# Optimization experiments

Hardware: AMD Instinct MI355X
Metric: run time of the kernel (lower is better)

Reference implementation:

```python
import jax, jax.numpy as jnp
import numpy as np

HID = 128
N_BLOCKS = 50000
ATOMS_PER_BLOCK = 8
N_ATOMS = N_BLOCKS * ATOMS_PER_BLOCK  # 400k
N_EDGES = 800000
ATOM_VOCAB = 100
N_BOND_TYPES = 5
CORRUPT_RATIO = 0.1


def setup_inputs() -> dict:
    key = jax.random.key(0)
    ks = jax.random.split(key, 20)
    A = jax.random.randint(ks[0], (N_ATOMS,), 0, ATOM_VOCAB)
    src = jax.random.randint(ks[1], (N_EDGES,), 0, N_ATOMS)
    dst = jax.random.randint(ks[2], (N_EDGES,), 0, N_ATOMS)
    btyp = jax.random.randint(ks[3], (N_EDGES,), 0, N_BOND_TYPES)
    bonds = jnp.stack([src, dst, btyp], axis=1)  # [E, 3]
    block_ids = jnp.arange(N_ATOMS) // ATOMS_PER_BLOCK  # atom -> block, sorted
    generate_mask = jax.random.uniform(ks[4], (N_BLOCKS,)) < 0.5
    position_ids = jax.random.randint(ks[5], (N_BLOCKS,), 0, 1024)
    is_aa = jax.random.randint(ks[6], (N_BLOCKS,), 0, 2)
    corrupt_rand = jax.random.uniform(ks[7], (N_BLOCKS,))
    s = 0.02
    p = {
        'atom_embed': jax.random.normal(ks[8], (ATOM_VOCAB, HID)) * s,
        'bond_embed': jax.random.normal(ks[9], (N_BOND_TYPES, HID)) * s,
        'is_aa_embed': jax.random.normal(ks[10], (2, HID)) * s,
        'gine_w1': jax.random.normal(ks[11], (HID, HID)) * s,
        'gine_b1': jnp.zeros((HID,)),
        'gine_w2': jax.random.normal(ks[12], (HID, HID)) * s,
        'gine_b2': jnp.zeros((HID,)),
        'mlp_w0': jax.random.normal(ks[13], (3 * HID, HID)) * s,
        'mlp_b0': jnp.zeros((HID,)),
        'mlp_w1': jax.random.normal(ks[14], (HID, HID)) * s,
        'mlp_b1': jnp.zeros((HID,)),
        'mlp_w2': jax.random.normal(ks[15], (HID, HID)) * s,
        'mlp_b2': jnp.zeros((HID,)),
    }
    return dict(A=A, bonds=bonds, block_ids=block_ids, generate_mask=generate_mask,
                position_ids=position_ids, is_aa=is_aa, corrupt_rand=corrupt_rand, **p)


def _sinusoidal(pos, dim):
    # standard sinusoidal position embedding, [N] -> [N, dim]
    inv_freq = 1.0 / (10000.0 ** (jnp.arange(0, dim, 2, dtype=jnp.float32) / dim))
    ang = pos.astype(jnp.float32)[:, None] * inv_freq[None, :]
    return jnp.concatenate([jnp.sin(ang), jnp.cos(ang)], axis=-1)


def reference(A, bonds, block_ids, generate_mask, position_ids, is_aa, corrupt_rand,
              atom_embed, bond_embed, is_aa_embed,
              gine_w1, gine_b1, gine_w2, gine_b2,
              mlp_w0, mlp_b0, mlp_w1, mlp_b1, mlp_w2, mlp_b2):
    src, dst, btyp = bonds[:, 0], bonds[:, 1], bonds[:, 2]
    # context atoms: atoms whose block is NOT being generated
    ctx = ~generate_mask[block_ids]                       # [N_atoms]
    valid = (ctx[src] & ctx[dst]).astype(jnp.float32)     # edge-select mask (== dropping bonds)
    # GINEConv: msg = relu(x_j + e), aggregated by sum at dst, eps = 0
    Hn = atom_embed[A]                                    # [N_atoms, H]
    edge_attr = bond_embed[btyp]                          # [E, H]
    msg = jax.nn.relu(Hn[src] + edge_attr) * valid[:, None]
    agg = jax.ops.segment_sum(msg, dst, num_segments=N_ATOMS)
    h = Hn + agg
    h = jax.nn.relu(h @ gine_w1 + gine_b1) @ gine_w2 + gine_b2
    # std-conserving scatter mean: sum / sqrt(count)
    blk_sum = jax.ops.segment_sum(h, block_ids, num_segments=N_BLOCKS)
    cnt = jax.ops.segment_sum(jnp.ones((N_ATOMS,), jnp.float32), block_ids, num_segments=N_BLOCKS)
    topo = blk_sum / jnp.sqrt(jnp.maximum(cnt, 1.0))[:, None]
    topo = jnp.where(generate_mask[:, None], 0.0, topo)
    # is_aa embedding with corruption on generated blocks
    corrupt = generate_mask & (corrupt_rand < CORRUPT_RATIO)
    is_aa_e = is_aa_embed[jnp.where(corrupt, 0, is_aa)]
    pos_e = _sinusoidal(position_ids, HID)
    x = jnp.concatenate([pos_e, topo, is_aa_e], axis=-1)  # [N_blocks, 3H]
    # 3-layer cond MLP (dropout inactive in eval)
    x = jax.nn.relu(x @ mlp_w0 + mlp_b0)
    x = jax.nn.relu(x @ mlp_w1 + mlp_b1)
    cond = x @ mlp_w2 + mlp_b2
    return cond
```

## Files before the change

kernel.cpp:

```cpp
#include <hip/hip_runtime.h>
#include <hip/hip_bf16.h>

#define NBLK  50000
#define NATOM 400000
#define NEDGE 800000
#define CAP   40

typedef __bf16 bf16x8 __attribute__((ext_vector_type(8)));
typedef float  f32x4  __attribute__((ext_vector_type(4)));

#define MCNT_OFF 0UL
#define EW1_OFF  200000UL
#define REC_OFF  251200UL
#define T_OFF    4251200UL
#define PW_OFF   4507200UL
#define W2T_OFF  4769344UL
#define M1T_OFF  4802112UL
#define M2T_OFF  4834880UL
#define AAW_OFF  4867648UL
#define GM_OFF   4869696UL
#define FLAG_OFF 4919696UL
#define TOPO_OFF 4919712UL
#define WS_NEED  18403840UL

#define RS8 0.35355339059327373f

#define MFMA(a,b,c) __builtin_amdgcn_mfma_f32_16x16x32_bf16((a),(b),(c),0,0,0)

__device__ inline f32x4 splat4(float v){ f32x4 r; r[0]=v; r[1]=v; r[2]=v; r[3]=v; return r; }
__device__ inline float scrub(float v){ return (v==v && v<1e30f && v>-1e30f) ? v : 0.f; }

__global__ void k_sniff(const void* gm_raw, char* ws) {
  __shared__ int big;
  if (threadIdx.x == 0) big = 0;
  __syncthreads();
  const unsigned* gw = (const unsigned*)gm_raw;
  for (int i = threadIdx.x; i < 12500; i += 256)
    if (gw[i] > 1u) big = 1;
  __syncthreads();
  if (threadIdx.x == 0) *(int*)(ws + FLAG_OFF) = big;
}

__global__ void k_prep(const float* atom_embed, const float* bond_embed,
                       const float* m0, const float* m1, const float* m2,
                       const float* g2, const float* gb2, const float* aa_embed,
                       const void* gm_raw, const int* __restrict__ bonds,
                       const int* __restrict__ A, char* ws) {
  int b = blockIdx.x, t = threadIdx.x;
  if (b < 100) {
    float ae = atom_embed[b*128 + t];
    float* T = (float*)(ws + T_OFF);
    for (int bo = 0; bo < 5; ++bo) {
      float v = ae + bond_embed[bo*128 + t];
      T[(b*5 + bo)*128 + t] = v > 0.f ? v : 0.f;
    }
  } else if (b < 116) {
    int wb = b - 100;
    const float* src; __bf16* dst; int r0;
    if (wb < 8) { src = m1; dst = (__bf16*)(ws + M1T_OFF); r0 = wb*16; }
    else        { src = m2; dst = (__bf16*)(ws + M2T_OFF); r0 = (wb-8)*16; }
    for (int rr = 0; rr < 16; ++rr) {
      int r = r0 + rr;
      dst[t*128 + r] = (__bf16)src[r*128 + t];
    }
  } else if (b < 166) {
    int anyBig = *(const int*)(ws + FLAG_OFF);
    int base = (b - 116) * 1000;
    unsigned char* gu = (unsigned char*)(ws + GM_OFF);
    if (anyBig) {
      const unsigned char* gb = (const unsigned char*)gm_raw;
      for (int i = t; i < 1000; i += 128) gu[base+i] = gb[base+i] ? 1 : 0;
    } else {
      const int* gi = (const int*)gm_raw;
      for (int i = t; i < 1000; i += 128) gu[base+i] = gi[base+i] ? 1 : 0;
    }
  } else if (b < 1190) {
    int p = b - 166;
    __shared__ float s[128];
    int c = t & 63;
    float invf = exp2f((float)c * -0.20762050593046012f);
    float ang = (float)p * invf;
    s[t] = (t < 64) ? __sinf(ang) : __cosf(ang);
    __syncthreads();
    float acc = 0.f;
    #pragma unroll 4
    for (int j = 0; j < 128; ++j) acc += s[j] * m0[j*128 + t];
    ((__bf16*)(ws + PW_OFF))[p*128 + t] = (__bf16)acc;
  } else if (b < 1318) {
    int r = b - 1190;
    float acc = 0.f;
    #pragma unroll 4
    for (int j = 0; j < 128; ++j) acc += g2[r*128 + j] * m0[(128+j)*128 + t];
    ((__bf16*)(ws + W2T_OFF))[t*128 + r] = (__bf16)(acc * RS8);
  } else if (b < 1322) {
    int sf = b - 1318, sel = sf & 1, f = sf >> 1;
    float acc = 0.f;
    #pragma unroll 4
    for (int j = 0; j < 128; ++j) acc += aa_embed[sel*128 + j] * m0[(256+j)*128 + t];
    if (f) {
      float cacc = 0.f;
      #pragma unroll 4
      for (int j = 0; j < 128; ++j) cacc += gb2[j] * m0[(128+j)*128 + t];
      acc += 8.0f * RS8 * cacc;
    }
    ((float*)(ws + AAW_OFF))[sf*128 + t] = acc;
  } else {
    int anyBig = *(const int*)(ws + FLAG_OFF);
    const unsigned char* g8 = (const unsigned char*)gm_raw;
    const int* g32 = (const int*)gm_raw;
    long base = ((long)(b - 1322)*128 + t)*8;
    #pragma unroll 2
    for (int h = 0; h < 2; ++h) {
      long e4 = base + h*4;
      if (e4 >= NEDGE) break;
      const int4* bp = (const int4*)(bonds + e4*3);
      int4 w0 = bp[0], w1 = bp[1], w2 = bp[2];
      int srcs[4] = {w0.x, w0.w, w1.z, w2.y};
      int dsts[4] = {w0.y, w1.x, w1.w, w2.z};
      int bts[4]  = {w0.z, w1.y, w2.x, w2.w};
      #pragma unroll
      for (int i = 0; i < 4; ++i) {
        int sm_ = srcs[i] >> 3, dm = dsts[i] >> 3;
        int bad = anyBig ? ((int)g8[sm_] | (int)g8[dm]) : (g32[sm_] | g32[dm]);
        if (bad) continue;
        int slot = atomicAdd((int*)(ws + MCNT_OFF) + dm, 1);
        if (slot >= 0 && slot < CAP)
          ((unsigned short*)(ws + REC_OFF))[dm*CAP + slot] =
            (unsigned short)((A[srcs[i]]*5 + bts[i])*8 + (dsts[i] & 7));
      }
    }
  }
}

__global__ void k_prep2(const float* atom_embed, const float* g1, const float* gb1,
                        char* ws) {
  int b = blockIdx.x, t = threadIdx.x;
  float s0 = 0.f, s1 = 0.f, s2 = 0.f, s3 = 0.f;
  const float* row = (b < 100) ? (atom_embed + b*128) : ((float*)(ws + T_OFF) + (b-100)*128);
  #pragma unroll 4
  for (int k = 0; k < 128; k += 4) {
    s0 += row[k+0] * g1[(k+0)*128 + t];
    s1 += row[k+1] * g1[(k+1)*128 + t];
    s2 += row[k+2] * g1[(k+2)*128 + t];
    s3 += row[k+3] * g1[(k+3)*128 + t];
  }
  float s = (s0 + s1) + (s2 + s3);
  if (b < 100) {
    ((float*)(ws + EW1_OFF))[b*128 + t] = s + gb1[t];
  } else {
    __syncthreads();
    ((float*)(ws + T_OFF))[(b-100)*128 + t] = s;
  }
}

__launch_bounds__(256, 6)
__global__ void k_gather5(char* ws, const int* __restrict__ A) {
  const int tid = threadIdx.x;
  const int lane = tid & 63, wid = tid >> 6;
  const int mol = blockIdx.x*4 + wid;
  const int a_l = lane >> 3, q8 = lane & 7;
  const unsigned char* gm = (const unsigned char*)(ws + GM_OFF);

  f32x4 a0 = splat4(0.f), a1 = splat4(0.f), a2 = splat4(0.f), a3 = splat4(0.f);
  f32x4 b0 = splat4(0.f), b1 = splat4(0.f), b2 = splat4(0.f), b3 = splat4(0.f);
  if (!gm[mol]) {
    const int* cnt = (const int*)(ws + MCNT_OFF);
    const unsigned* rec32 = (const unsigned*)(ws + REC_OFF);
    const unsigned short* rec16 = (const unsigned short*)(ws + REC_OFF);
    const float* EW1 = (const float*)(ws + EW1_OFF);
    const float* TW1 = (const float*)(ws + T_OFF);
    int n = cnt[mol];
    if (n > CAP) n = CAP;
    if (n < 0) n = 0;
    int aT = A[mol*8 + a_l];
    const f32x4* ep = (const f32x4*)(EW1 + aT*128 + q8*16);
    a0 = ep[0]; a1 = ep[1]; a2 = ep[2]; a3 = ep[3];
    const int base32 = mol*(CAP/2);
    int i = 0;
    for (; i + 4 <= n; i += 4) {
      unsigned pr0 = rec32[base32 + (i >> 1)];
      unsigned pr1 = rec32[base32 + (i >> 1) + 1];
      int rv0 = pr0 & 0xFFFF, rv1 = pr0 >> 16;
      int rv2 = pr1 & 0xFFFF, rv3 = pr1 >> 16;
      int p0 = rv0 >> 3, p1 = rv1 >> 3, p2 = rv2 >> 3, p3 = rv3 >> 3;
      if (p0 < 500 && (rv0 & 7) == a_l) {
        const f32x4* tp = (const f32x4*)(TW1 + p0*128 + q8*16);
        a0 += tp[0]; a1 += tp[1]; a2 += tp[2]; a3 += tp[3];
      }
      if (p1 < 500 && (rv1 & 7) == a_l) {
        const f32x4* tp = (const f32x4*)(TW1 + p1*128 + q8*16);
        b0 += tp[0]; b1 += tp[1]; b2 += tp[2]; b3 += tp[3];
      }
      if (p2 < 500 && (rv2 & 7) == a_l) {
        const f32x4* tp = (const f32x4*)(TW1 + p2*128 + q8*16);
        a0 += tp[0]; a1 += tp[1]; a2 += tp[2]; a3 += tp[3];
      }
      if (p3 < 500 && (rv3 & 7) == a_l) {
        const f32x4* tp = (const f32x4*)(TW1 + p3*128 + q8*16);
        b0 += tp[0]; b1 += tp[1]; b2 += tp[2]; b3 += tp[3];
      }
    }
    for (; i < n; ++i) {
      int rv = rec16[mol*CAP + i];
      int p = rv >> 3;
      if (p < 500 && (rv & 7) == a_l) {
        const f32x4* tp = (const f32x4*)(TW1 + p*128 + q8*16);
        b0 += tp[0]; b1 += tp[1]; b2 += tp[2]; b3 += tp[3];
      }
    }
  }
  #pragma unroll
  for (int k = 0; k < 4; ++k) {
    float x0 = fmaxf(a0[k] + b0[k], 0.f), x1 = fmaxf(a1[k] + b1[k], 0.f);
    float x2 = fmaxf(a2[k] + b2[k], 0.f), x3 = fmaxf(a3[k] + b3[k], 0.f);
    x0 += __shfl_xor(x0, 8);  x1 += __shfl_xor(x1, 8);
    x2 += __shfl_xor(x2, 8);  x3 += __shfl_xor(x3, 8);
    x0 += __shfl_xor(x0, 16); x1 += __shfl_xor(x1, 16);
    x2 += __shfl_xor(x2, 16); x3 += __shfl_xor(x3, 16);
    x0 += __shfl_xor(x0, 32); x1 += __shfl_xor(x1, 32);
    x2 += __shfl_xor(x2, 32); x3 += __shfl_xor(x3, 32);
    a0[k] = x0; a1[k] = x1; a2[k] = x2; a3[k] = x3;
  }
  if (a_l == 0) {
    bf16x8 o0, o1;
    #pragma unroll
    for (int k = 0; k < 4; ++k) {
      o0[k] = (__bf16)a0[k]; o0[k+4] = (__bf16)a1[k];
      o1[k] = (__bf16)a2[k]; o1[k+4] = (__bf16)a3[k];
    }
    char* dst = ws + TOPO_OFF + (long)mol*256 + q8*32;
    *(bf16x8*)dst = o0;
    *(bf16x8*)(dst + 16) = o1;
  }
}

__device__ inline void gemm4(const char* sm, int aoff, const __bf16* wt,
                             const float* bias, int lane, int wave, f32x4 acc[4][2]) {
  const int colA = wave*32 + (lane & 15);
  const int k0   = (lane >> 4) * 8;
  float bb0 = bias[colA], bb1 = bias[colA + 16];
  #pragma unroll
  for (int m = 0; m < 4; ++m) { acc[m][0] = splat4(bb0); acc[m][1] = splat4(bb1); }
  #pragma unroll
  for (int kb = 0; kb < 4; ++kb) {
    bf16x8 b0 = *(const bf16x8*)(wt + colA*128 + kb*32 + k0);
    bf16x8 b1 = *(const bf16x8*)(wt + (colA+16)*128 + kb*32 + k0);
    #pragma unroll
    for (int m = 0; m < 4; ++m) {
      int rA = m*16 + (lane & 15);
      int byte = aoff + rA*256 + (((kb*64) + k0*2) ^ ((rA & 7) << 4));
      bf16x8 a = *(const bf16x8*)(sm + byte);
      acc[m][0] = MFMA(a, b0, acc[m][0]);
      acc[m][1] = MFMA(a, b1, acc[m][1]);
    }
  }
}

__device__ inline void stor4(char* sm, int off, f32x4 acc[4][2],
                             int lane, int wave, bool do_relu) {
  #pragma unroll
  for (int m = 0; m < 4; ++m)
  #pragma unroll
  for (int nf = 0; nf < 2; ++nf)
  #pragma unroll
  for (int r = 0; r < 4; ++r) {
    float v = acc[m][nf][r];
    if (do_relu && v < 0.f) v = 0.f;
    int row = m*16 + (lane >> 4)*4 + r;
    int col = wave*32 + nf*16 + (lane & 15);
    int byte = off + row*256 + ((col*2) ^ ((row & 7) << 4));
    *(__bf16*)(sm + byte) = (__bf16)v;
  }
}

__launch_bounds__(256)
__global__ void k_mlp3(char* ws, const int* __restrict__ pos_ids,
                       const int* __restrict__ is_aa, const float* cr,
                       const float* mb0, const float* mb1, const float* mb2,
                       float* __restrict__ out) {
  __shared__ __align__(16) char sm[32768];
  const int tid = threadIdx.x, lane = tid & 63, wave = tid >> 6;
  const int r0 = blockIdx.x * 64;
  const unsigned char* gm = (const unsigned char*)(ws + GM_OFF);
  const __bf16* topo_pre = (const __bf16*)(ws + TOPO_OFF);

  for (int i = 0; i < 4; ++i) {
    int idx = tid + i*256;
    int row = idx >> 4, c = idx & 15;
    int mol = r0 + row;
    bf16x8 v;
    #pragma unroll
    for (int j = 0; j < 8; ++j) v[j] = (__bf16)0.f;
    if (mol < NBLK) v = *(const bf16x8*)(topo_pre + (long)mol*128 + c*8);
    int byte = row*256 + ((c*16) ^ ((row & 7) << 4));
    *(bf16x8*)(sm + byte) = v;
  }
  if (tid < 64) {
    int mol = r0 + tid, packed = 0;
    if (mol < NBLK) {
      int g = gm[mol];
      int corrupt = g && (cr[mol] < 0.1f);
      int sel = corrupt ? 0 : is_aa[mol];
      packed = pos_ids[mol] | (sel << 12) | ((g ? 0 : 1) << 13);
    }
    *(int*)(sm + 16384 + tid*4) = packed;
  }
  __syncthreads();

  f32x4 acc[4][2];
  gemm4(sm, 0, (const __bf16*)(ws + W2T_OFF), mb0, lane, wave, acc);
  {
    const __bf16* PW = (const __bf16*)(ws + PW_OFF);
    const float* AAW = (const float*)(ws + AAW_OFF);
    #pragma unroll
    for (int m = 0; m < 4; ++m)
    #pragma unroll
    for (int r = 0; r < 4; ++r) {
      int row = m*16 + (lane >> 4)*4 + r;
      int packed = *(const int*)(sm + 16384 + row*4);
      int pid = packed & 0xFFF, sf = (packed >> 12) & 3;
      #pragma unroll
      for (int nf = 0; nf < 2; ++nf) {
        int col = wave*32 + nf*16 + (lane & 15);
        float v = acc[m][nf][r] + (float)PW[pid*128 + col] + AAW[sf*128 + col];
        acc[m][nf][r] = fmaxf(v, 0.f);
      }
    }
  }
  __syncthreads();
  stor4(sm, 0, acc, lane, wave, false);
  __syncthreads();

  gemm4(sm, 0, (const __bf16*)(ws + M1T_OFF), mb1, lane, wave, acc);
  stor4(sm, 16384, acc, lane, wave, true);
  __syncthreads();

  gemm4(sm, 16384, (const __bf16*)(ws + M2T_OFF), mb2, lane, wave, acc);
  #pragma unroll
  for (int m = 0; m < 4; ++m)
  #pragma unroll
  for (int nf = 0; nf < 2; ++nf)
  #pragma unroll
  for (int r = 0; r < 4; ++r) {
    int row = m*16 + (lane >> 4)*4 + r;
    int col = wave*32 + nf*16 + (lane & 15);
    int mol = r0 + row;
    if (mol < NBLK) out[(long)mol*128 + col] = scrub(acc[m][nf][r]);
  }
}

extern "C" void kernel_launch(void* const* d_in, const int* in_sizes, int n_in,
                              void* d_out, int out_size, void* d_ws, size_t ws_size,
                              hipStream_t stream) {
  if (ws_size < WS_NEED) return;
  const int* A      = (const int*)d_in[0];
  const int* bonds  = (const int*)d_in[1];
  const void* gm    = d_in[3];
  const int* pos    = (const int*)d_in[4];
  const int* isaa   = (const int*)d_in[5];
  const float* cr   = (const float*)d_in[6];
  const float* atom_embed = (const float*)d_in[7];
  const float* bond_embed = (const float*)d_in[8];
  const float* aa_embed   = (const float*)d_in[9];
  const float* g1  = (const float*)d_in[10];
  const float* gb1 = (const float*)d_in[11];
  const float* g2  = (const float*)d_in[12];
  const float* gb2 = (const float*)d_in[13];
  const float* m0  = (const float*)d_in[14];
  const float* mb0 = (const float*)d_in[15];
  const float* m1  = (const float*)d_in[16];
  const float* mb1 = (const float*)d_in[17];
  const float* m2  = (const float*)d_in[18];
  const float* mb2 = (const float*)d_in[19];
  char* ws = (char*)d_ws;

  hipMemsetAsync(ws + MCNT_OFF, 0, (size_t)NBLK*4, stream);
  k_sniff  <<<1, 256, 0, stream>>>(gm, ws);
  k_prep   <<<2104, 128, 0, stream>>>(atom_embed, bond_embed, m0, m1, m2,
                                      g2, gb2, aa_embed, gm, bonds, A, ws);
  k_prep2  <<<600, 128, 0, stream>>>(atom_embed, g1, gb1, ws);
  k_gather5<<<NBLK/4, 256, 0, stream>>>(ws, A);
  k_mlp3   <<<(NBLK + 63)/64, 256, 0, stream>>>(ws, pos, isaa, cr,
                                                mb0, mb1, mb2, (float*)d_out);
}
```

Baseline: 113.8 us.

## Move MLP weight precompute into gather kernel and process two molecules per wave

New measurement: 120.2 us. +5.6%, slower.

```diff
diff --git a/kernel.cpp b/kernel.cpp
--- a/kernel.cpp
+++ b/kernel.cpp
@@ -42,8 +42,7 @@
 }
 
 __global__ void k_prep(const float* atom_embed, const float* bond_embed,
-                       const float* m0, const float* m1, const float* m2,
-                       const float* g2, const float* gb2, const float* aa_embed,
+                       const float* m1, const float* m2,
                        const void* gm_raw, const int* __restrict__ bonds,
                        const int* __restrict__ A, char* ws) {
   int b = blockIdx.x, t = threadIdx.x;
@@ -74,41 +73,11 @@
       const int* gi = (const int*)gm_raw;
       for (int i = t; i < 1000; i += 128) gu[base+i] = gi[base+i] ? 1 : 0;
     }
-  } else if (b < 1190) {
-    int p = b - 166;
-    __shared__ float s[128];
-    int c = t & 63;
-    float invf = exp2f((float)c * -0.20762050593046012f);
-    float ang = (float)p * invf;
-    s[t] = (t < 64) ? __sinf(ang) : __cosf(ang);
-    __syncthreads();
-    float acc = 0.f;
-    #pragma unroll 4
-    for (int j = 0; j < 128; ++j) acc += s[j] * m0[j*128 + t];
-    ((__bf16*)(ws + PW_OFF))[p*128 + t] = (__bf16)acc;
-  } else if (b < 1318) {
-    int r = b - 1190;
-    float acc = 0.f;
-    #pragma unroll 4
-    for (int j = 0; j < 128; ++j) acc += g2[r*128 + j] * m0[(128+j)*128 + t];
-    ((__bf16*)(ws + W2T_OFF))[t*128 + r] = (__bf16)(acc * RS8);
-  } else if (b < 1322) {
-    int sf = b - 1318, sel = sf & 1, f = sf >> 1;
-    float acc = 0.f;
-    #pragma unroll 4
-    for (int j = 0; j < 128; ++j) acc += aa_embed[sel*128 + j] * m0[(256+j)*128 + t];
-    if (f) {
-      float cacc = 0.f;
-      #pragma unroll 4
-      for (int j = 0; j < 128; ++j) cacc += gb2[j] * m0[(128+j)*128 + t];
-      acc += 8.0f * RS8 * cacc;
-    }
-    ((float*)(ws + AAW_OFF))[sf*128 + t] = acc;
   } else {
     int anyBig = *(const int*)(ws + FLAG_OFF);
     const unsigned char* g8 = (const unsigned char*)gm_raw;
     const int* g32 = (const int*)gm_raw;
-    long base = ((long)(b - 1322)*128 + t)*8;
+    long base = ((long)(b - 166)*128 + t)*8;
     #pragma unroll 2
     for (int h = 0; h < 2; ++h) {
       long e4 = base + h*4;
@@ -153,84 +122,146 @@
   }
 }
 
-__launch_bounds__(256, 6)
-__global__ void k_gather5(char* ws, const int* __restrict__ A) {
-  const int tid = threadIdx.x;
-  const int lane = tid & 63, wid = tid >> 6;
-  const int mol = blockIdx.x*4 + wid;
-  const int a_l = lane >> 3, q8 = lane & 7;
-  const unsigned char* gm = (const unsigned char*)(ws + GM_OFF);
-
-  f32x4 a0 = splat4(0.f), a1 = splat4(0.f), a2 = splat4(0.f), a3 = splat4(0.f);
-  f32x4 b0 = splat4(0.f), b1 = splat4(0.f), b2 = splat4(0.f), b3 = splat4(0.f);
-  if (!gm[mol]) {
+__launch_bounds__(256, 4)
+__global__ void k_gather6(char* ws, const int* __restrict__ A,
+                          const float* __restrict__ m0w, const float* __restrict__ g2,
+                          const float* __restrict__ gb2, const float* __restrict__ aa_embed) {
+  const int b = blockIdx.x, t = threadIdx.x;
+  if (b < 6250) {
+    const int lane = t & 63, wid = t >> 6;
+    const int molA = b*8 + wid*2, molB = molA + 1;
+    const int a_l = lane >> 3, q8 = lane & 7;
+    const unsigned char* gm = (const unsigned char*)(ws + GM_OFF);
     const int* cnt = (const int*)(ws + MCNT_OFF);
     const unsigned* rec32 = (const unsigned*)(ws + REC_OFF);
     const unsigned short* rec16 = (const unsigned short*)(ws + REC_OFF);
     const float* EW1 = (const float*)(ws + EW1_OFF);
     const float* TW1 = (const float*)(ws + T_OFF);
-    int n = cnt[mol];
-    if (n > CAP) n = CAP;
-    if (n < 0) n = 0;
-    int aT = A[mol*8 + a_l];
-    const f32x4* ep = (const f32x4*)(EW1 + aT*128 + q8*16);
-    a0 = ep[0]; a1 = ep[1]; a2 = ep[2]; a3 = ep[3];
-    const int base32 = mol*(CAP/2);
-    int i = 0;
-    for (; i + 4 <= n; i += 4) {
-      unsigned pr0 = rec32[base32 + (i >> 1)];
-      unsigned pr1 = rec32[base32 + (i >> 1) + 1];
-      int rv0 = pr0 & 0xFFFF, rv1 = pr0 >> 16;
-      int rv2 = pr1 & 0xFFFF, rv3 = pr1 >> 16;
-      int p0 = rv0 >> 3, p1 = rv1 >> 3, p2 = rv2 >> 3, p3 = rv3 >> 3;
-      if (p0 < 500 && (rv0 & 7) == a_l) {
-        const f32x4* tp = (const f32x4*)(TW1 + p0*128 + q8*16);
-        a0 += tp[0]; a1 += tp[1]; a2 += tp[2]; a3 += tp[3];
-      }
-      if (p1 < 500 && (rv1 & 7) == a_l) {
-        const f32x4* tp = (const f32x4*)(TW1 + p1*128 + q8*16);
-        b0 += tp[0]; b1 += tp[1]; b2 += tp[2]; b3 += tp[3];
-      }
-      if (p2 < 500 && (rv2 & 7) == a_l) {
-        const f32x4* tp = (const f32x4*)(TW1 + p2*128 + q8*16);
-        a0 += tp[0]; a1 += tp[1]; a2 += tp[2]; a3 += tp[3];
-      }
-      if (p3 < 500 && (rv3 & 7) == a_l) {
-        const f32x4* tp = (const f32x4*)(TW1 + p3*128 + q8*16);
-        b0 += tp[0]; b1 += tp[1]; b2 += tp[2]; b3 += tp[3];
-      }
-    }
-    for (; i < n; ++i) {
-      int rv = rec16[mol*CAP + i];
+
+    int gmA = gm[molA], gmB = gm[molB];
+    int cA = cnt[molA], cB = cnt[molB];
+    int aTA = A[molA*8 + a_l], aTB = A[molB*8 + a_l];
+    const f32x4* epA = (const f32x4*)(EW1 + aTA*128 + q8*16);
+    const f32x4* epB = (const f32x4*)(EW1 + aTB*128 + q8*16);
+    f32x4 A0 = epA[0], A1 = epA[1], A2 = epA[2], A3 = epA[3];
+    f32x4 B0 = epB[0], B1 = epB[1], B2 = epB[2], B3 = epB[3];
+    int nA = gmA ? 0 : (cA < 0 ? 0 : (cA > CAP ? CAP : cA));
+    int nB = gmB ? 0 : (cB < 0 ? 0 : (cB > CAP ? CAP : cB));
+    if (gmA) { A0 = splat4(0.f); A1 = A0; A2 = A0; A3 = A0; }
+    if (gmB) { B0 = splat4(0.f); B1 = B0; B2 = B0; B3 = B0; }
+
+    for (int i = 0; (i + 2 <= nA) | (i + 2 <= nB); i += 2) {
+      if (i + 2 <= nA) {
+        unsigned pr = rec32[molA*20 + (i >> 1)];
+        int rv0 = pr & 0xFFFF, rv1 = pr >> 16;
+        int p0 = rv0 >> 3, p1 = rv1 >> 3;
+        if (p0 < 500 && (rv0 & 7) == a_l) {
+          const f32x4* tp = (const f32x4*)(TW1 + p0*128 + q8*16);
+          A0 += tp[0]; A1 += tp[1]; A2 += tp[2]; A3 += tp[3];
+        }
+        if (p1 < 500 && (rv1 & 7) == a_l) {
+          const f32x4* tp = (const f32x4*)(TW1 + p1*128 + q8*16);
+          A0 += tp[0]; A1 += tp[1]; A2 += tp[2]; A3 += tp[3];
+        }
+      }
+      if (i + 2 <= nB) {
+        unsigned pr = rec32[molB*20 + (i >> 1)];
+        int rv0 = pr & 0xFFFF, rv1 = pr >> 16;
+        int p0 = rv0 >> 3, p1 = rv1 >> 3;
+        if (p0 < 500 && (rv0 & 7) == a_l) {
+          const f32x4* tp = (const f32x4*)(TW1 + p0*128 + q8*16);
+          B0 += tp[0]; B1 += tp[1]; B2 += tp[2]; B3 += tp[3];
+        }
+        if (p1 < 500 && (rv1 & 7) == a_l) {
+          const f32x4* tp = (const f32x4*)(TW1 + p1*128 + q8*16);
+          B0 += tp[0]; B1 += tp[1]; B2 += tp[2]; B3 += tp[3];
+        }
+      }
+    }
+    if (nA & 1) {
+      int rv = rec16[molA*CAP + nA - 1];
       int p = rv >> 3;
       if (p < 500 && (rv & 7) == a_l) {
         const f32x4* tp = (const f32x4*)(TW1 + p*128 + q8*16);
-        b0 += tp[0]; b1 += tp[1]; b2 += tp[2]; b3 += tp[3];
-      }
-    }
-  }
-  #pragma unroll
-  for (int k = 0; k < 4; ++k) {
-    float x0 = fmaxf(a0[k] + b0[k], 0.f), x1 = fmaxf(a1[k] + b1[k], 0.f);
-    float x2 = fmaxf(a2[k] + b2[k], 0.f), x3 = fmaxf(a3[k] + b3[k], 0.f);
-    x0 += __shfl_xor(x0, 8);  x1 += __shfl_xor(x1, 8);
-    x2 += __shfl_xor(x2, 8);  x3 += __shfl_xor(x3, 8);
-    x0 += __shfl_xor(x0, 16); x1 += __shfl_xor(x1, 16);
-    x2 += __shfl_xor(x2, 16); x3 += __shfl_xor(x3, 16);
-    x0 += __shfl_xor(x0, 32); x1 += __shfl_xor(x1, 32);
-    x2 += __shfl_xor(x2, 32); x3 += __shfl_xor(x3, 32);
-    a0[k] = x0; a1[k] = x1; a2[k] = x2; a3[k] = x3;
-  }
-  if (a_l == 0) {
-    bf16x8 o0, o1;
+        A0 += tp[0]; A1 += tp[1]; A2 += tp[2]; A3 += tp[3];
+      }
+    }
+    if (nB & 1) {
+      int rv = rec16[molB*CAP + nB - 1];
+      int p = rv >> 3;
+      if (p < 500 && (rv & 7) == a_l) {
+        const f32x4* tp = (const f32x4*)(TW1 + p*128 + q8*16);
+        B0 += tp[0]; B1 += tp[1]; B2 += tp[2]; B3 += tp[3];
+      }
+    }
     #pragma unroll
     for (int k = 0; k < 4; ++k) {
-      o0[k] = (__bf16)a0[k]; o0[k+4] = (__bf16)a1[k];
-      o1[k] = (__bf16)a2[k]; o1[k+4] = (__bf16)a3[k];
-    }
-    char* dst = ws + TOPO_OFF + (long)mol*256 + q8*32;
-    *(bf16x8*)dst = o0;
-    *(bf16x8*)(dst + 16) = o1;
+      float xa0 = fmaxf(A0[k], 0.f), xa1 = fmaxf(A1[k], 0.f);
+      float xa2 = fmaxf(A2[k], 0.f), xa3 = fmaxf(A3[k], 0.f);
+      float xb0 = fmaxf(B0[k], 0.f), xb1 = fmaxf(B1[k], 0.f);
+      float xb2 = fmaxf(B2[k], 0.f), xb3 = fmaxf(B3[k], 0.f);
+      xa0 += __shfl_xor(xa0, 8);  xa1 += __shfl_xor(xa1, 8);
+      xa2 += __shfl_xor(xa2, 8);  xa3 += __shfl_xor(xa3, 8);
+      xb0 += __shfl_xor(xb0, 8);  xb1 += __shfl_xor(xb1, 8);
+      xb2 += __shfl_xor(xb2, 8);  xb3 += __shfl_xor(xb3, 8);
+      xa0 += __shfl_xor(xa0, 16); xa1 += __shfl_xor(xa1, 16);
+      xa2 += __shfl_xor(xa2, 16); xa3 += __shfl_xor(xa3, 16);
+      xb0 += __shfl_xor(xb0, 16); xb1 += __shfl_xor(xb1, 16);
+      xb2 += __shfl_xor(xb2, 16); xb3 += __shfl_xor(xb3, 16);
+      xa0 += __shfl_xor(xa0, 32); xa1 += __shfl_xor(xa1, 32);
+      xa2 += __shfl_xor(xa2, 32); xa3 += __shfl_xor(xa3, 32);
+      xb0 += __shfl_xor(xb0, 32); xb1 += __shfl_xor(xb1, 32);
+      xb2 += __shfl_xor(xb2, 32); xb3 += __shfl_xor(xb3, 32);
+      A0[k] = xa0; A1[k] = xa1; A2[k] = xa2; A3[k] = xa3;
+      B0[k] = xb0; B1[k] = xb1; B2[k] = xb2; B3[k] = xb3;
+    }
+    if (a_l == 0) {
+      bf16x8 oA0, oA1, oB0, oB1;
+      #pragma unroll
+      for (int k = 0; k < 4; ++k) {
+        oA0[k] = (__bf16)A0[k]; oA0[k+4] = (__bf16)A1[k];
+        oA1[k] = (__bf16)A2[k]; oA1[k+4] = (__bf16)A3[k];
+        oB0[k] = (__bf16)B0[k]; oB0[k+4] = (__bf16)B1[k];
+        oB1[k] = (__bf16)B2[k]; oB1[k+4] = (__bf16)B3[k];
+      }
+      char* dA = ws + TOPO_OFF + (long)molA*256 + q8*32;
+      char* dB = ws + TOPO_OFF + (long)molB*256 + q8*32;
+      *(bf16x8*)dA = oA0; *(bf16x8*)(dA + 16) = oA1;
+      *(bf16x8*)dB = oB0; *(bf16x8*)(dB + 16) = oB1;
+    }
+  } else if (b < 6762) {
+    __shared__ float s[256];
+    int half = t >> 7, tt = t & 127;
+    int p = (b - 6250)*2 + half;
+    int c = tt & 63;
+    float invf = exp2f((float)c * -0.20762050593046012f);
+    float ang = (float)p * invf;
+    s[half*128 + tt] = (tt < 64) ? __sinf(ang) : __cosf(ang);
+    __syncthreads();
+    float acc = 0.f;
+    #pragma unroll 4
+    for (int j = 0; j < 128; ++j) acc += s[half*128 + j] * m0w[j*128 + tt];
+    ((__bf16*)(ws + PW_OFF))[p*128 + tt] = (__bf16)acc;
+  } else if (b < 6826) {
+    int half = t >> 7, tt = t & 127;
+    int r = (b - 6762)*2 + half;
+    float acc = 0.f;
+    #pragma unroll 4
+    for (int j = 0; j < 128; ++j) acc += g2[r*128 + j] * m0w[(128+j)*128 + tt];
+    ((__bf16*)(ws + W2T_OFF))[tt*128 + r] = (__bf16)(acc * RS8);
+  } else {
+    int half = t >> 7, tt = t & 127;
+    int sf = (b - 6826)*2 + half, sel = sf & 1, f = sf >> 1;
+    float acc = 0.f;
+    #pragma unroll 4
+    for (int j = 0; j < 128; ++j) acc += aa_embed[sel*128 + j] * m0w[(256+j)*128 + tt];
+    if (f) {
+      float cacc = 0.f;
+      #pragma unroll 4
+      for (int j = 0; j < 128; ++j) cacc += gb2[j] * m0w[(128+j)*128 + tt];
+      acc += 8.0f * RS8 * cacc;
+    }
+    ((float*)(ws + AAW_OFF))[sf*128 + tt] = acc;
   }
 }
 
@@ -376,10 +407,10 @@
 
   hipMemsetAsync(ws + MCNT_OFF, 0, (size_t)NBLK*4, stream);
   k_sniff  <<<1, 256, 0, stream>>>(gm, ws);
-  k_prep   <<<2104, 128, 0, stream>>>(atom_embed, bond_embed, m0, m1, m2,
-                                      g2, gb2, aa_embed, gm, bonds, A, ws);
+  k_prep   <<<948, 128, 0, stream>>>(atom_embed, bond_embed, m1, m2,
+                                     gm, bonds, A, ws);
   k_prep2  <<<600, 128, 0, stream>>>(atom_embed, g1, gb1, ws);
-  k_gather5<<<NBLK/4, 256, 0, stream>>>(ws, A);
+  k_gather6<<<6828, 256, 0, stream>>>(ws, A, m0, g2, gb2, aa_embed);
   k_mlp3   <<<(NBLK + 63)/64, 256, 0, stream>>>(ws, pos, isaa, cr,
                                                 mb0, mb1, mb2, (float*)d_out);
 }
```

## Process four molecules per wave in gather kernel to raise memory-level parallelism

Applied to the files above, without the earlier changes.

Measured after the change: 133.8 us. +17.5%, slower.

```diff
diff --git a/kernel.cpp b/kernel.cpp
--- a/kernel.cpp
+++ b/kernel.cpp
@@ -153,84 +153,130 @@
   }
 }
 
-__launch_bounds__(256, 6)
-__global__ void k_gather5(char* ws, const int* __restrict__ A) {
+#define EDGE_HIT(RV, ACCA, ACCB)                                            \
+  { int p_ = (RV) >> 3;                                                     \
+    if (p_ < 500 && ((RV) & 7) == a_l) {                                    \
+      const f32x4* tp_ = (const f32x4*)(TW1 + p_*128 + q8*16);              \
+      ACCA##0 += tp_[0]; ACCA##1 += tp_[1];                                 \
+      ACCB##2 += tp_[2]; ACCB##3 += tp_[3]; } }
+
+__launch_bounds__(256, 3)
+__global__ void k_gather7(char* ws, const int* __restrict__ A) {
   const int tid = threadIdx.x;
   const int lane = tid & 63, wid = tid >> 6;
-  const int mol = blockIdx.x*4 + wid;
+  const int mol0 = (blockIdx.x*4 + wid)*4;
   const int a_l = lane >> 3, q8 = lane & 7;
   const unsigned char* gm = (const unsigned char*)(ws + GM_OFF);
-
-  f32x4 a0 = splat4(0.f), a1 = splat4(0.f), a2 = splat4(0.f), a3 = splat4(0.f);
-  f32x4 b0 = splat4(0.f), b1 = splat4(0.f), b2 = splat4(0.f), b3 = splat4(0.f);
-  if (!gm[mol]) {
-    const int* cnt = (const int*)(ws + MCNT_OFF);
-    const unsigned* rec32 = (const unsigned*)(ws + REC_OFF);
-    const unsigned short* rec16 = (const unsigned short*)(ws + REC_OFF);
-    const float* EW1 = (const float*)(ws + EW1_OFF);
-    const float* TW1 = (const float*)(ws + T_OFF);
-    int n = cnt[mol];
-    if (n > CAP) n = CAP;
-    if (n < 0) n = 0;
-    int aT = A[mol*8 + a_l];
-    const f32x4* ep = (const f32x4*)(EW1 + aT*128 + q8*16);
-    a0 = ep[0]; a1 = ep[1]; a2 = ep[2]; a3 = ep[3];
-    const int base32 = mol*(CAP/2);
-    int i = 0;
-    for (; i + 4 <= n; i += 4) {
-      unsigned pr0 = rec32[base32 + (i >> 1)];
-      unsigned pr1 = rec32[base32 + (i >> 1) + 1];
-      int rv0 = pr0 & 0xFFFF, rv1 = pr0 >> 16;
-      int rv2 = pr1 & 0xFFFF, rv3 = pr1 >> 16;
-      int p0 = rv0 >> 3, p1 = rv1 >> 3, p2 = rv2 >> 3, p3 = rv3 >> 3;
-      if (p0 < 500 && (rv0 & 7) == a_l) {
-        const f32x4* tp = (const f32x4*)(TW1 + p0*128 + q8*16);
-        a0 += tp[0]; a1 += tp[1]; a2 += tp[2]; a3 += tp[3];
-      }
-      if (p1 < 500 && (rv1 & 7) == a_l) {
-        const f32x4* tp = (const f32x4*)(TW1 + p1*128 + q8*16);
-        b0 += tp[0]; b1 += tp[1]; b2 += tp[2]; b3 += tp[3];
-      }
-      if (p2 < 500 && (rv2 & 7) == a_l) {
-        const f32x4* tp = (const f32x4*)(TW1 + p2*128 + q8*16);
-        a0 += tp[0]; a1 += tp[1]; a2 += tp[2]; a3 += tp[3];
-      }
-      if (p3 < 500 && (rv3 & 7) == a_l) {
-        const f32x4* tp = (const f32x4*)(TW1 + p3*128 + q8*16);
-        b0 += tp[0]; b1 += tp[1]; b2 += tp[2]; b3 += tp[3];
-      }
-    }
-    for (; i < n; ++i) {
-      int rv = rec16[mol*CAP + i];
-      int p = rv >> 3;
-      if (p < 500 && (rv & 7) == a_l) {
-        const f32x4* tp = (const f32x4*)(TW1 + p*128 + q8*16);
-        b0 += tp[0]; b1 += tp[1]; b2 += tp[2]; b3 += tp[3];
-      }
-    }
-  }
+  const int* cnt = (const int*)(ws + MCNT_OFF);
+  const unsigned* rec32 = (const unsigned*)(ws + REC_OFF);
+  const unsigned short* rec16 = (const unsigned short*)(ws + REC_OFF);
+  const float* EW1 = (const float*)(ws + EW1_OFF);
+  const float* TW1 = (const float*)(ws + T_OFF);
+
+  unsigned g4 = *(const unsigned*)(gm + mol0);
+  int4 c4 = *(const int4*)(cnt + mol0);
+  int aT0 = A[(mol0+0)*8 + a_l];
+  int aT1 = A[(mol0+1)*8 + a_l];
+  int aT2 = A[(mol0+2)*8 + a_l];
+  int aT3 = A[(mol0+3)*8 + a_l];
+  int m0_ = g4 & 255, m1_ = (g4 >> 8) & 255, m2_ = (g4 >> 16) & 255, m3_ = g4 >> 24;
+  int n0 = m0_ ? 0 : (c4.x < 0 ? 0 : (c4.x > CAP ? CAP : c4.x));
+  int n1 = m1_ ? 0 : (c4.y < 0 ? 0 : (c4.y > CAP ? CAP : c4.y));
+  int n2 = m2_ ? 0 : (c4.z < 0 ? 0 : (c4.z > CAP ? CAP : c4.z));
+  int n3 = m3_ ? 0 : (c4.w < 0 ? 0 : (c4.w > CAP ? CAP : c4.w));
+
+  const f32x4* ep0 = (const f32x4*)(EW1 + aT0*128 + q8*16);
+  const f32x4* ep1 = (const f32x4*)(EW1 + aT1*128 + q8*16);
+  const f32x4* ep2 = (const f32x4*)(EW1 + aT2*128 + q8*16);
+  const f32x4* ep3 = (const f32x4*)(EW1 + aT3*128 + q8*16);
+  f32x4 A0 = ep0[0], A1 = ep0[1], A2 = ep0[2], A3 = ep0[3];
+  f32x4 B0 = ep1[0], B1 = ep1[1], B2 = ep1[2], B3 = ep1[3];
+  f32x4 C0 = ep2[0], C1 = ep2[1], C2 = ep2[2], C3 = ep2[3];
+  f32x4 D0 = ep3[0], D1 = ep3[1], D2 = ep3[2], D3 = ep3[3];
+  if (m0_) { A0 = splat4(0.f); A1 = A0; A2 = A0; A3 = A0; }
+  if (m1_) { B0 = splat4(0.f); B1 = B0; B2 = B0; B3 = B0; }
+  if (m2_) { C0 = splat4(0.f); C1 = C0; C2 = C0; C3 = C0; }
+  if (m3_) { D0 = splat4(0.f); D1 = D0; D2 = D0; D3 = D0; }
+
+  int nmax = n0 > n1 ? n0 : n1;
+  nmax = nmax > n2 ? nmax : n2;
+  nmax = nmax > n3 ? nmax : n3;
+  for (int i = 0; i + 2 <= nmax; i += 2) {
+    if (i + 2 <= n0) {
+      unsigned pr = rec32[(mol0+0)*20 + (i >> 1)];
+      int rv0 = pr & 0xFFFF, rv1 = pr >> 16;
+      EDGE_HIT(rv0, A, A); EDGE_HIT(rv1, A, A);
+    }
+    if (i + 2 <= n1) {
+      unsigned pr = rec32[(mol0+1)*20 + (i >> 1)];
+      int rv0 = pr & 0xFFFF, rv1 = pr >> 16;
+      EDGE_HIT(rv0, B, B); EDGE_HIT(rv1, B, B);
+    }
+    if (i + 2 <= n2) {
+      unsigned pr = rec32[(mol0+2)*20 + (i >> 1)];
+      int rv0 = pr & 0xFFFF, rv1 = pr >> 16;
+      EDGE_HIT(rv0, C, C); EDGE_HIT(rv1, C, C);
+    }
+    if (i + 2 <= n3) {
+      unsigned pr = rec32[(mol0+3)*20 + (i >> 1)];
+      int rv0 = pr & 0xFFFF, rv1 = pr >> 16;
+      EDGE_HIT(rv0, D, D); EDGE_HIT(rv1, D, D);
+    }
+  }
+  if (n0 & 1) { int rv = rec16[(mol0+0)*CAP + n0 - 1]; EDGE_HIT(rv, A, A); }
+  if (n1 & 1) { int rv = rec16[(mol0+1)*CAP + n1 - 1]; EDGE_HIT(rv, B, B); }
+  if (n2 & 1) { int rv = rec16[(mol0+2)*CAP + n2 - 1]; EDGE_HIT(rv, C, C); }
+  if (n3 & 1) { int rv = rec16[(mol0+3)*CAP + n3 - 1]; EDGE_HIT(rv, D, D); }
+
   #pragma unroll
   for (int k = 0; k < 4; ++k) {
-    float x0 = fmaxf(a0[k] + b0[k], 0.f), x1 = fmaxf(a1[k] + b1[k], 0.f);
-    float x2 = fmaxf(a2[k] + b2[k], 0.f), x3 = fmaxf(a3[k] + b3[k], 0.f);
-    x0 += __shfl_xor(x0, 8);  x1 += __shfl_xor(x1, 8);
-    x2 += __shfl_xor(x2, 8);  x3 += __shfl_xor(x3, 8);
-    x0 += __shfl_xor(x0, 16); x1 += __shfl_xor(x1, 16);
-    x2 += __shfl_xor(x2, 16); x3 += __shfl_xor(x3, 16);
-    x0 += __shfl_xor(x0, 32); x1 += __shfl_xor(x1, 32);
-    x2 += __shfl_xor(x2, 32); x3 += __shfl_xor(x3, 32);
-    a0[k] = x0; a1[k] = x1; a2[k] = x2; a3[k] = x3;
+    float xa0 = fmaxf(A0[k], 0.f), xa1 = fmaxf(A1[k], 0.f);
+    float xa2 = fmaxf(A2[k], 0.f), xa3 = fmaxf(A3[k], 0.f);
+    float xb0 = fmaxf(B0[k], 0.f), xb1 = fmaxf(B1[k], 0.f);
+    float xb2 = fmaxf(B2[k], 0.f), xb3 = fmaxf(B3[k], 0.f);
+    float xc0 = fmaxf(C0[k], 0.f), xc1 = fmaxf(C1[k], 0.f);
+    float xc2 = fmaxf(C2[k], 0.f), xc3 = fmaxf(C3[k], 0.f);
+    float xd0 = fmaxf(D0[k], 0.f), xd1 = fmaxf(D1[k], 0.f);
+    float xd2 = fmaxf(D2[k], 0.f), xd3 = fmaxf(D3[k], 0.f);
+    #pragma unroll
+    for (int d = 8; d <= 32; d <<= 1) {
+      xa0 += __shfl_xor(xa0, d); xa1 += __shfl_xor(xa1, d);
+      xa2 += __shfl_xor(xa2, d); xa3 += __shfl_xor(xa3, d);
+      xb0 += __shfl_xor(xb0, d); xb1 += __shfl_xor(xb1, d);
+      xb2 += __shfl_xor(xb2, d); xb3 += __shfl_xor(xb3, d);
+      xc0 += __shfl_xor(xc0, d); xc1 += __shfl_xor(xc1, d);
+      xc2 += __shfl_xor(xc2, d); xc3 += __shfl_xor(xc3, d);
+      xd0 += __shfl_xor(xd0, d); xd1 += __shfl_xor(xd1, d);
+      xd2 += __shfl_xor(xd2, d); xd3 += __shfl_xor(xd3, d);
+    }
+    A0[k] = xa0; A1[k] = xa1; A2[k] = xa2; A3[k] = xa3;
+    B0[k] = xb0; B1[k] = xb1; B2[k] = xb2; B3[k] = xb3;
+    C0[k] = xc0; C1[k] = xc1; C2[k] = xc2; C3[k] = xc3;
+    D0[k] = xd0; D1[k] = xd1; D2[k] = xd2; D3[k] = xd3;
   }
   if (a_l == 0) {
     bf16x8 o0, o1;
-    #pragma unroll
-    for (int k = 0; k < 4; ++k) {
-      o0[k] = (__bf16)a0[k]; o0[k+4] = (__bf16)a1[k];
-      o1[k] = (__bf16)a2[k]; o1[k+4] = (__bf16)a3[k];
-    }
-    char* dst = ws + TOPO_OFF + (long)mol*256 + q8*32;
-    *(bf16x8*)dst = o0;
-    *(bf16x8*)(dst + 16) = o1;
+    char* dst;
+    #pragma unroll
+    for (int k = 0; k < 4; ++k) { o0[k] = (__bf16)A0[k]; o0[k+4] = (__bf16)A1[k];
+                                  o1[k] = (__bf16)A2[k]; o1[k+4] = (__bf16)A3[k]; }
+    dst = ws + TOPO_OFF + (long)(mol0+0)*256 + q8*32;
+    *(bf16x8*)dst = o0; *(bf16x8*)(dst + 16) = o1;
+    #pragma unroll
+    for (int k = 0; k < 4; ++k) { o0[k] = (__bf16)B0[k]; o0[k+4] = (__bf16)B1[k];
+                                  o1[k] = (__bf16)B2[k]; o1[k+4] = (__bf16)B3[k]; }
+    dst = ws + TOPO_OFF + (long)(mol0+1)*256 + q8*32;
+    *(bf16x8*)dst = o0; *(bf16x8*)(dst + 16) = o1;
+    #pragma unroll
+    for (int k = 0; k < 4; ++k) { o0[k] = (__bf16)C0[k]; o0[k+4] = (__bf16)C1[k];
+                                  o1[k] = (__bf16)C2[k]; o1[k+4] = (__bf16)C3[k]; }
+    dst = ws + TOPO_OFF + (long)(mol0+2)*256 + q8*32;
+    *(bf16x8*)dst = o0; *(bf16x8*)(dst + 16) = o1;
+    #pragma unroll
+    for (int k = 0; k < 4; ++k) { o0[k] = (__bf16)D0[k]; o0[k+4] = (__bf16)D1[k];
+                                  o1[k] = (__bf16)D2[k]; o1[k+4] = (__bf16)D3[k]; }
+    dst = ws + TOPO_OFF + (long)(mol0+3)*256 + q8*32;
+    *(bf16x8*)dst = o0; *(bf16x8*)(dst + 16) = o1;
   }
 }
 
@@ -379,7 +425,7 @@
   k_prep   <<<2104, 128, 0, stream>>>(atom_embed, bond_embed, m0, m1, m2,
                                       g2, gb2, aa_embed, gm, bonds, A, ws);
   k_prep2  <<<600, 128, 0, stream>>>(atom_embed, g1, gb1, ws);
-  k_gather5<<<NBLK/4, 256, 0, stream>>>(ws, A);
+  k_gather7<<<3125, 256, 0, stream>>>(ws, A);
   k_mlp3   <<<(NBLK + 63)/64, 256, 0, stream>>>(ws, pos, isaa, cr,
                                                 mb0, mb1, mb2, (float*)d_out);
 }
```

## Make MLP waves independent over 16-row tiles and parallelize dtype sniff

Applied to the files above, without the earlier changes.

Measured after the change: 136.9 us. +20.3%, slower.

```diff
diff --git a/kernel.cpp b/kernel.cpp
--- a/kernel.cpp
+++ b/kernel.cpp
@@ -31,14 +31,9 @@
 __device__ inline float scrub(float v){ return (v==v && v<1e30f && v>-1e30f) ? v : 0.f; }
 
 __global__ void k_sniff(const void* gm_raw, char* ws) {
-  __shared__ int big;
-  if (threadIdx.x == 0) big = 0;
-  __syncthreads();
+  int i = blockIdx.x*256 + threadIdx.x;
   const unsigned* gw = (const unsigned*)gm_raw;
-  for (int i = threadIdx.x; i < 12500; i += 256)
-    if (gw[i] > 1u) big = 1;
-  __syncthreads();
-  if (threadIdx.x == 0) *(int*)(ws + FLAG_OFF) = big;
+  if (i < 12500 && gw[i] > 1u) atomicOr((int*)(ws + FLAG_OFF), 1);
 }
 
 __global__ void k_prep(const float* atom_embed, const float* bond_embed,
@@ -234,118 +229,126 @@
   }
 }
 
-__device__ inline void gemm4(const char* sm, int aoff, const __bf16* wt,
-                             const float* bias, int lane, int wave, f32x4 acc[4][2]) {
-  const int colA = wave*32 + (lane & 15);
-  const int k0   = (lane >> 4) * 8;
-  float bb0 = bias[colA], bb1 = bias[colA + 16];
-  #pragma unroll
-  for (int m = 0; m < 4; ++m) { acc[m][0] = splat4(bb0); acc[m][1] = splat4(bb1); }
-  #pragma unroll
-  for (int kb = 0; kb < 4; ++kb) {
-    bf16x8 b0 = *(const bf16x8*)(wt + colA*128 + kb*32 + k0);
-    bf16x8 b1 = *(const bf16x8*)(wt + (colA+16)*128 + kb*32 + k0);
-    #pragma unroll
-    for (int m = 0; m < 4; ++m) {
-      int rA = m*16 + (lane & 15);
-      int byte = aoff + rA*256 + (((kb*64) + k0*2) ^ ((rA & 7) << 4));
-      bf16x8 a = *(const bf16x8*)(sm + byte);
-      acc[m][0] = MFMA(a, b0, acc[m][0]);
-      acc[m][1] = MFMA(a, b1, acc[m][1]);
-    }
-  }
-}
-
-__device__ inline void stor4(char* sm, int off, f32x4 acc[4][2],
-                             int lane, int wave, bool do_relu) {
-  #pragma unroll
-  for (int m = 0; m < 4; ++m)
-  #pragma unroll
-  for (int nf = 0; nf < 2; ++nf)
-  #pragma unroll
-  for (int r = 0; r < 4; ++r) {
-    float v = acc[m][nf][r];
-    if (do_relu && v < 0.f) v = 0.f;
-    int row = m*16 + (lane >> 4)*4 + r;
-    int col = wave*32 + nf*16 + (lane & 15);
-    int byte = off + row*256 + ((col*2) ^ ((row & 7) << 4));
-    *(__bf16*)(sm + byte) = (__bf16)v;
-  }
-}
-
-__launch_bounds__(256)
-__global__ void k_mlp3(char* ws, const int* __restrict__ pos_ids,
+__global__ void k_mlp4(char* ws, const int* __restrict__ pos_ids,
                        const int* __restrict__ is_aa, const float* cr,
                        const float* mb0, const float* mb1, const float* mb2,
                        float* __restrict__ out) {
-  __shared__ __align__(16) char sm[32768];
-  const int tid = threadIdx.x, lane = tid & 63, wave = tid >> 6;
-  const int r0 = blockIdx.x * 64;
+  __shared__ __align__(16) char sm[16384];
+  const int tid = threadIdx.x, lane = tid & 63, wid = tid >> 6;
+  const int m0r = blockIdx.x*64 + wid*16;
+  char* wl = sm + wid*4096;
+  const int rA = lane & 15;
+  const int k8 = (lane >> 4) * 8;
+
   const unsigned char* gm = (const unsigned char*)(ws + GM_OFF);
-  const __bf16* topo_pre = (const __bf16*)(ws + TOPO_OFF);
-
-  for (int i = 0; i < 4; ++i) {
-    int idx = tid + i*256;
-    int row = idx >> 4, c = idx & 15;
-    int mol = r0 + row;
-    bf16x8 v;
+  int pid[4], sf[4];
+  #pragma unroll
+  for (int j = 0; j < 4; ++j) {
+    int mol = m0r + (lane >> 4)*4 + j;
+    if (mol >= NBLK) mol = NBLK - 1;
+    int g = gm[mol];
+    int corrupt = g && (cr[mol] < 0.1f);
+    pid[j] = pos_ids[mol];
+    sf[j] = (corrupt ? 0 : is_aa[mol]) + ((g ? 0 : 1) << 1);
+  }
+
+  const __bf16* topo = (const __bf16*)(ws + TOPO_OFF);
+  int aMol = m0r + rA;
+  if (aMol >= NBLK) aMol = NBLK - 1;
+  bf16x8 at0 = *(const bf16x8*)(topo + (long)aMol*128 +   0 + k8);
+  bf16x8 at1 = *(const bf16x8*)(topo + (long)aMol*128 +  32 + k8);
+  bf16x8 at2 = *(const bf16x8*)(topo + (long)aMol*128 +  64 + k8);
+  bf16x8 at3 = *(const bf16x8*)(topo + (long)aMol*128 +  96 + k8);
+
+  const __bf16* W2T = (const __bf16*)(ws + W2T_OFF);
+  const __bf16* M1T = (const __bf16*)(ws + M1T_OFF);
+  const __bf16* M2T = (const __bf16*)(ws + M2T_OFF);
+  const __bf16* PW  = (const __bf16*)(ws + PW_OFF);
+  const float*  AAW = (const float*)(ws + AAW_OFF);
+  f32x4 acc[8];
+
+  #pragma unroll
+  for (int cb = 0; cb < 8; ++cb) acc[cb] = splat4(mb0[cb*16 + rA]);
+  #pragma unroll
+  for (int cb = 0; cb < 8; ++cb) {
+    bf16x8 bf0 = *(const bf16x8*)(W2T + (cb*16 + rA)*128 +   0 + k8);
+    bf16x8 bf1 = *(const bf16x8*)(W2T + (cb*16 + rA)*128 +  32 + k8);
+    bf16x8 bf2 = *(const bf16x8*)(W2T + (cb*16 + rA)*128 +  64 + k8);
+    bf16x8 bf3 = *(const bf16x8*)(W2T + (cb*16 + rA)*128 +  96 + k8);
+    acc[cb] = MFMA(at0, bf0, acc[cb]);
+    acc[cb] = MFMA(at1, bf1, acc[cb]);
+    acc[cb] = MFMA(at2, bf2, acc[cb]);
+    acc[cb] = MFMA(at3, bf3, acc[cb]);
+  }
+  #pragma unroll
+  for (int cb = 0; cb < 8; ++cb) {
+    int col = cb*16 + rA;
     #pragma unroll
-    for (int j = 0; j < 8; ++j) v[j] = (__bf16)0.f;
-    if (mol < NBLK) v = *(const bf16x8*)(topo_pre + (long)mol*128 + c*8);
-    int byte = row*256 + ((c*16) ^ ((row & 7) << 4));
-    *(bf16x8*)(sm + byte) = v;
-  }
-  if (tid < 64) {
-    int mol = r0 + tid, packed = 0;
-    if (mol < NBLK) {
-      int g = gm[mol];
-      int corrupt = g && (cr[mol] < 0.1f);
-      int sel = corrupt ? 0 : is_aa[mol];
-      packed = pos_ids[mol] | (sel << 12) | ((g ? 0 : 1) << 13);
-    }
-    *(int*)(sm + 16384 + tid*4) = packed;
-  }
-  __syncthreads();
-
-  f32x4 acc[4][2];
-  gemm4(sm, 0, (const __bf16*)(ws + W2T_OFF), mb0, lane, wave, acc);
-  {
-    const __bf16* PW = (const __bf16*)(ws + PW_OFF);
-    const float* AAW = (const float*)(ws + AAW_OFF);
+    for (int j = 0; j < 4; ++j) {
+      int row = (lane >> 4)*4 + j;
+      float v = acc[cb][j] + (float)PW[pid[j]*128 + col] + AAW[sf[j]*128 + col];
+      v = fmaxf(v, 0.f);
+      *(__bf16*)(wl + row*256 + ((col*2) ^ ((row & 7) << 4))) = (__bf16)v;
+    }
+  }
+  asm volatile("s_waitcnt lgkmcnt(0)" ::: "memory");
+
+  bf16x8 ah0 = *(const bf16x8*)(wl + rA*256 + ((  0 + k8*2) ^ ((rA & 7) << 4)));
+  bf16x8 ah1 = *(const bf16x8*)(wl + rA*256 + (( 64 + k8*2) ^ ((rA & 7) << 4)));
+  bf16x8 ah2 = *(const bf16x8*)(wl + rA*256 + ((128 + k8*2) ^ ((rA & 7) << 4)));
+  bf16x8 ah3 = *(const bf16x8*)(wl + rA*256 + ((192 + k8*2) ^ ((rA & 7) << 4)));
+  #pragma unroll
+  for (int cb = 0; cb < 8; ++cb) acc[cb] = splat4(mb1[cb*16 + rA]);
+  #pragma unroll
+  for (int cb = 0; cb < 8; ++cb) {
+    bf16x8 bf0 = *(const bf16x8*)(M1T + (cb*16 + rA)*128 +   0 + k8);
+    bf16x8 bf1 = *(const bf16x8*)(M1T + (cb*16 + rA)*128 +  32 + k8);
+    bf16x8 bf2 = *(const bf16x8*)(M1T + (cb*16 + rA)*128 +  64 + k8);
+    bf16x8 bf3 = *(const bf16x8*)(M1T + (cb*16 + rA)*128 +  96 + k8);
+    acc[cb] = MFMA(ah0, bf0, acc[cb]);
+    acc[cb] = MFMA(ah1, bf1, acc[cb]);
+    acc[cb] = MFMA(ah2, bf2, acc[cb]);
+    acc[cb] = MFMA(ah3, bf3, acc[cb]);
+  }
+  asm volatile("s_waitcnt lgkmcnt(0)" ::: "memory");
+  #pragma unroll
+  for (int cb = 0; cb < 8; ++cb) {
+    int col = cb*16 + rA;
     #pragma unroll
-    for (int m = 0; m < 4; ++m)
+    for (int j = 0; j < 4; ++j) {
+      int row = (lane >> 4)*4 + j;
+      float v = fmaxf(acc[cb][j], 0.f);
+      *(__bf16*)(wl + row*256 + ((col*2) ^ ((row & 7) << 4))) = (__bf16)v;
+    }
+  }
+  asm volatile("s_waitcnt lgkmcnt(0)" ::: "memory");
+
+  ah0 = *(const bf16x8*)(wl + rA*256 + ((  0 + k8*2) ^ ((rA & 7) << 4)));
+  ah1 = *(const bf16x8*)(wl + rA*256 + (( 64 + k8*2) ^ ((rA & 7) << 4)));
+  ah2 = *(const bf16x8*)(wl + rA*256 + ((128 + k8*2) ^ ((rA & 7) << 4)));
+  ah3 = *(const bf16x8*)(wl + rA*256 + ((192 + k8*2) ^ ((rA & 7) << 4)));
+  #pragma unroll
+  for (int cb = 0; cb < 8; ++cb) acc[cb] = splat4(mb2[cb*16 + rA]);
+  #pragma unroll
+  for (int cb = 0; cb < 8; ++cb) {
+    bf16x8 bf0 = *(const bf16x8*)(M2T + (cb*16 + rA)*128 +   0 + k8);
+    bf16x8 bf1 = *(const bf16x8*)(M2T + (cb*16 + rA)*128 +  32 + k8);
+    bf16x8 bf2 = *(const bf16x8*)(M2T + (cb*16 + rA)*128 +  64 + k8);
+    bf16x8 bf3 = *(const bf16x8*)(M2T + (cb*16 + rA)*128 +  96 + k8);
+    acc[cb] = MFMA(ah0, bf0, acc[cb]);
+    acc[cb] = MFMA(ah1, bf1, acc[cb]);
+    acc[cb] = MFMA(ah2, bf2, acc[cb]);
+    acc[cb] = MFMA(ah3, bf3, acc[cb]);
+  }
+  #pragma unroll
+  for (int cb = 0; cb < 8; ++cb) {
+    int col = cb*16 + rA;
     #pragma unroll
-    for (int r = 0; r < 4; ++r) {
-      int row = m*16 + (lane >> 4)*4 + r;
-      int packed = *(const int*)(sm + 16384 + row*4);
-      int pid = packed & 0xFFF, sf = (packed >> 12) & 3;
-      #pragma unroll
-      for (int nf = 0; nf < 2; ++nf) {
-        int col = wave*32 + nf*16 + (lane & 15);
-        float v = acc[m][nf][r] + (float)PW[pid*128 + col] + AAW[sf*128 + col];
-        acc[m][nf][r] = fmaxf(v, 0.f);
-      }
-    }
-  }
-  __syncthreads();
-  stor4(sm, 0, acc, lane, wave, false);
-  __syncthreads();
-
-  gemm4(sm, 0, (const __bf16*)(ws + M1T_OFF), mb1, lane, wave, acc);
-  stor4(sm, 16384, acc, lane, wave, true);
-  __syncthreads();
-
-  gemm4(sm, 16384, (const __bf16*)(ws + M2T_OFF), mb2, lane, wave, acc);
-  #pragma unroll
-  for (int m = 0; m < 4; ++m)
-  #pragma unroll
-  for (int nf = 0; nf < 2; ++nf)
-  #pragma unroll
-  for (int r = 0; r < 4; ++r) {
-    int row = m*16 + (lane >> 4)*4 + r;
-    int col = wave*32 + nf*16 + (lane & 15);
-    int mol = r0 + row;
-    if (mol < NBLK) out[(long)mol*128 + col] = scrub(acc[m][nf][r]);
+    for (int j = 0; j < 4; ++j) {
+      int row = (lane >> 4)*4 + j;
+      int mol = m0r + row;
+      if (mol < NBLK) out[(long)mol*128 + col] = scrub(acc[cb][j]);
+    }
   }
 }
 
@@ -375,11 +378,12 @@
   char* ws = (char*)d_ws;
 
   hipMemsetAsync(ws + MCNT_OFF, 0, (size_t)NBLK*4, stream);
-  k_sniff  <<<1, 256, 0, stream>>>(gm, ws);
+  hipMemsetAsync(ws + FLAG_OFF, 0, 4, stream);
+  k_sniff  <<<49, 256, 0, stream>>>(gm, ws);
   k_prep   <<<2104, 128, 0, stream>>>(atom_embed, bond_embed, m0, m1, m2,
                                       g2, gb2, aa_embed, gm, bonds, A, ws);
   k_prep2  <<<600, 128, 0, stream>>>(atom_embed, g1, gb1, ws);
   k_gather5<<<NBLK/4, 256, 0, stream>>>(ws, A);
-  k_mlp3   <<<(NBLK + 63)/64, 256, 0, stream>>>(ws, pos, isaa, cr,
+  k_mlp4   <<<(NBLK + 63)/64, 256, 0, stream>>>(ws, pos, isaa, cr,
                                                 mb0, mb1, mb2, (float*)d_out);
 }
```
